# Kernel optimization log

Hardware: AMD Instinct MI355X
Metric: run time of the kernel (lower is better)

## Reference

```python
import jax, jax.numpy as jnp
import numpy as np

VOCAB, EMBED, HIDDEN = 32000, 256, 1024
B, T = 64, 256


def setup_inputs() -> dict:
    key = jax.random.key(0)
    ks = jax.random.split(key, 8)
    s = 0.05
    return {
        "x": jax.random.randint(ks[0], (B, T), 0, VOCAB),
        "embed_table": jax.random.normal(ks[1], (VOCAB, EMBED), jnp.float32) * s,
        "W_ih": jax.random.normal(ks[2], (4 * HIDDEN, EMBED), jnp.float32) * s,
        "W_hh": jax.random.normal(ks[3], (4 * HIDDEN, HIDDEN), jnp.float32) * s,
        "b_ih": jax.random.normal(ks[4], (4 * HIDDEN,), jnp.float32) * s,
        "b_hh": jax.random.normal(ks[5], (4 * HIDDEN,), jnp.float32) * s,
        "fc_W": jax.random.normal(ks[6], (VOCAB, HIDDEN), jnp.float32) * s,
        "fc_b": jax.random.normal(ks[7], (VOCAB,), jnp.float32) * s,
    }


def _lstm_last_hidden(emb, W_ih, W_hh, b_ih, b_hh):
    # emb: [B, T, E]. PyTorch gate order: i, f, g, o.
    H = W_hh.shape[1]
    # Precompute input-side gate projections for all steps: [T, B, 4H]
    x_gates = jnp.einsum('bte,ge->tbg', emb, W_ih) + (b_ih + b_hh)

    def step(carry, xg):
        h, c = carry
        z = xg + h @ W_hh.T  # [B, 4H]
        i = jax.nn.sigmoid(z[:, 0 * H:1 * H])
        f = jax.nn.sigmoid(z[:, 1 * H:2 * H])
        g = jnp.tanh(z[:, 2 * H:3 * H])
        o = jax.nn.sigmoid(z[:, 3 * H:4 * H])
        c = f * c + i * g
        h = o * jnp.tanh(c)
        return (h, c), None

    bsz = emb.shape[0]
    h0 = jnp.zeros((bsz, H), emb.dtype)
    (h, _), _ = jax.lax.scan(step, (h0, h0), x_gates)
    return h  # last hidden state [B, H]


def reference(x, embed_table, W_ih, W_hh, b_ih, b_hh, fc_W, fc_b):
    emb = embed_table[x]  # [B, T, E]
    h_last = _lstm_last_hidden(emb, W_ih, W_hh, b_ih, b_hh)
    return h_last @ fc_W.T + fc_b  # [B, VOCAB]
```

## Files before the change

### kernel.cpp

```cpp
#include <hip/hip_runtime.h>
#include <hip/hip_bf16.h>

#define VOCAB  32000
#define EMBED  256
#define HIDDEN 1024
#define G4     4096
#define BATCH  64
#define SEQ    256

typedef short s16x8 __attribute__((ext_vector_type(8)));
typedef float f32x4 __attribute__((ext_vector_type(4)));

static __device__ __forceinline__ unsigned short f2bf(float f) {
    unsigned u = __float_as_uint(f);
    unsigned r = (u + 0x7fffu + ((u >> 16) & 1u)) >> 16;
    return (unsigned short)r;
}
static __device__ __forceinline__ float bf2f(unsigned short s) {
    return __uint_as_float(((unsigned)s) << 16);
}

__global__ __launch_bounds__(256) void lstm_wprep(
    const float* __restrict__ W_hh,
    unsigned short* __restrict__ Wf)
{
    const int tile = blockIdx.x;
    const int ky   = blockIdx.y;
    const int tid  = threadIdx.x;
    const int wv   = tid >> 6;
    const int lane = tid & 63;
    const int ks   = ky * 4 + wv;
    const int r    = lane & 15;
    const int g    = lane >> 4;
    const int grow = (r >> 2) * 1024 + tile * 4 + (r & 3);
    const float* src = W_hh + (long)grow * 1024 + ks * 32 + g * 8;

    s16x8 hi, lo;
#pragma unroll
    for (int e = 0; e < 8; ++e) {
        const float v = src[e];
        const unsigned short h = f2bf(v);
        hi[e] = (short)h;
        lo[e] = (short)f2bf(v - bf2f(h));
    }
    s16x8* dst = (s16x8*)(Wf + ((long)(tile * 32 + ks) * 2) * 512) + lane;
    dst[0]  = hi;
    dst[64] = lo;
}

__global__ __launch_bounds__(256) void lstm_xgates(
    const int* __restrict__ x,
    const float* __restrict__ emb,
    const float* __restrict__ W_ih,
    const float* __restrict__ b_ih,
    const float* __restrict__ b_hh,
    float* __restrict__ xgT)
{
    const int t   = blockIdx.y;
    const int n0  = blockIdx.x * 64;
    const int tid = threadIdx.x;
    const int ty  = tid >> 4;
    const int tx  = tid & 15;

    __shared__ float As[64][36];
    __shared__ float Bs[64][36];
    __shared__ int   ridx[64];

    if (tid < 64) ridx[tid] = x[tid * SEQ + t];
    __syncthreads();

    float acc[4][4];
#pragma unroll
    for (int i = 0; i < 4; ++i)
#pragma unroll
        for (int j = 0; j < 4; ++j) acc[i][j] = 0.f;

    const int lr = tid >> 2;
    const int lc = (tid & 3) * 8;
    const float* abase = W_ih + (long)(n0 + lr) * EMBED + lc;
    const float* bbase = emb + (long)ridx[lr] * EMBED + lc;

    for (int k0 = 0; k0 < EMBED; k0 += 32) {
        *(float4*)&As[lr][lc]     = *(const float4*)(abase + k0);
        *(float4*)&As[lr][lc + 4] = *(const float4*)(abase + k0 + 4);
        *(float4*)&Bs[lr][lc]     = *(const float4*)(bbase + k0);
        *(float4*)&Bs[lr][lc + 4] = *(const float4*)(bbase + k0 + 4);
        __syncthreads();

#pragma unroll
        for (int kk = 0; kk < 32; kk += 4) {
            float4 av[4], bv[4];
#pragma unroll
            for (int i = 0; i < 4; ++i) av[i] = *(const float4*)&As[ty + 16 * i][kk];
#pragma unroll
            for (int j = 0; j < 4; ++j) bv[j] = *(const float4*)&Bs[tx + 16 * j][kk];
#pragma unroll
            for (int i = 0; i < 4; ++i)
#pragma unroll
                for (int j = 0; j < 4; ++j)
                    acc[i][j] += av[i].x * bv[j].x + av[i].y * bv[j].y
                               + av[i].z * bv[j].z + av[i].w * bv[j].w;
        }
        __syncthreads();
    }

#pragma unroll
    for (int i = 0; i < 4; ++i) {
        const int n = n0 + ty + 16 * i;
        const float bias = b_ih[n] + b_hh[n];
#pragma unroll
        for (int j = 0; j < 4; ++j) {
            const int b = tx + 16 * j;
            xgT[((long)t * G4 + n) * BATCH + b] = acc[i][j] + bias;
        }
    }
}

__global__ void lstm_init(float* __restrict__ c,
                          unsigned short* __restrict__ hhi,
                          unsigned short* __restrict__ hlo)
{
    const int i = blockIdx.x * blockDim.x + threadIdx.x;
    if (i < BATCH * HIDDEN) { c[i] = 0.f; hhi[i] = 0; hlo[i] = 0; }
}

__global__ __launch_bounds__(512, 1) void lstm_step(
    const unsigned short* __restrict__ Wf,
    const float* __restrict__ xgT_t,
    const unsigned short* __restrict__ hHi_in,
    const unsigned short* __restrict__ hLo_in,
    unsigned short* __restrict__ hHi_out,
    unsigned short* __restrict__ hLo_out,
    float* __restrict__ c)
{
    const int tile = blockIdx.x;
    const int tid  = threadIdx.x;
    const int w    = __builtin_amdgcn_readfirstlane(tid >> 6);
    const int lane = tid & 63;
    const int r16  = lane & 15;
    const int g    = lane >> 4;

    __shared__ float Zs[8 * 16 * 66];

    const s16x8* Wf8 = (const s16x8*)Wf;
    const s16x8* hh8 = (const s16x8*)hHi_in;
    const s16x8* hl8 = (const s16x8*)hLo_in;

    s16x8 Whi[4], Wlo[4];
#pragma unroll
    for (int s = 0; s < 4; ++s) {
        const long bi = ((long)(tile * 32 + w * 4 + s) * 2) * 64 + lane;
        Whi[s] = Wf8[bi];
        Wlo[s] = Wf8[bi + 64];
    }

    float xgv[4] = {0.f, 0.f, 0.f, 0.f};
    if (w < 4) {
#pragma unroll
        for (int gg = 0; gg < 4; ++gg)
            xgv[gg] = xgT_t[((long)(gg << 10) + (tile << 2) + w) * BATCH + lane];
    }

    f32x4 acc[4];
#pragma unroll
    for (int m = 0; m < 4; ++m) acc[m] = (f32x4){0.f, 0.f, 0.f, 0.f};

    s16x8 ah[2][4], al[2][4];
#pragma unroll
    for (int m = 0; m < 4; ++m) {
        const int hidx = (m * 16 + r16) * 128 + (w * 4) * 4 + g;
        ah[0][m] = hh8[hidx];
        al[0][m] = hl8[hidx];
    }

#pragma unroll
    for (int s = 0; s < 4; ++s) {
        const int cur = s & 1, nxt = cur ^ 1;
        if (s < 3) {
#pragma unroll
            for (int m = 0; m < 4; ++m) {
                const int hidx = (m * 16 + r16) * 128 + (w * 4 + s + 1) * 4 + g;
                ah[nxt][m] = hh8[hidx];
                al[nxt][m] = hl8[hidx];
            }
        }
#pragma unroll
        for (int m = 0; m < 4; ++m) {
            acc[m] = __builtin_amdgcn_mfma_f32_16x16x32_bf16(ah[cur][m], Whi[s], acc[m], 0, 0, 0);
            acc[m] = __builtin_amdgcn_mfma_f32_16x16x32_bf16(al[cur][m], Whi[s], acc[m], 0, 0, 0);
            acc[m] = __builtin_amdgcn_mfma_f32_16x16x32_bf16(ah[cur][m], Wlo[s], acc[m], 0, 0, 0);
        }
    }

#pragma unroll
    for (int m = 0; m < 4; ++m)
#pragma unroll
        for (int q = 0; q < 4; ++q) {
            const int b = m * 16 + g * 4 + q;
            Zs[(w * 16 + r16) * 66 + b] = acc[m][q];
        }
    __syncthreads();

    if (w < 4) {
        const int jj = w;
        const int b  = lane;
        float z[4];
#pragma unroll
        for (int gg = 0; gg < 4; ++gg) {
            float sum = xgv[gg];
#pragma unroll
            for (int wp = 0; wp < 8; ++wp)
                sum += Zs[(wp * 16 + gg * 4 + jj) * 66 + b];
            z[gg] = sum;
        }
        const float ig = 1.f / (1.f + __expf(-z[0]));
        const float fg = 1.f / (1.f + __expf(-z[1]));
        const float gt = tanhf(z[2]);
        const float og = 1.f / (1.f + __expf(-z[3]));
        float* cp = c + (tile * 64 + b) * 4 + jj;
        const float cn = fg * (*cp) + ig * gt;
        *cp = cn;
        const float hn = og * tanhf(cn);
        const unsigned short hhi = f2bf(hn);
        const unsigned short hlo = f2bf(hn - bf2f(hhi));
        hHi_out[b * HIDDEN + tile * 4 + jj] = hhi;
        hLo_out[b * HIDDEN + tile * 4 + jj] = hlo;
    }
}

__global__ __launch_bounds__(256) void lstm_fc(
    const unsigned short* __restrict__ h_hi,
    const unsigned short* __restrict__ h_lo,
    const float* __restrict__ fc_W,
    const float* __restrict__ fc_b,
    float* __restrict__ out)
{
    const int v0  = blockIdx.x * 64;
    const int tid = threadIdx.x;
    const int ty  = tid >> 4;
    const int tx  = tid & 15;

    __shared__ float Hs[64][36];
    __shared__ float Ws[64][36];

    float acc[4][4];
#pragma unroll
    for (int i = 0; i < 4; ++i)
#pragma unroll
        for (int j = 0; j < 4; ++j) acc[i][j] = 0.f;

    const int lr = tid >> 2;
    const int lc = (tid & 3) * 8;
    const s16x8* hi8 = (const s16x8*)h_hi;
    const s16x8* lo8 = (const s16x8*)h_lo;
    const float* wbase = fc_W + (long)(v0 + lr) * HIDDEN + lc;

    for (int k0 = 0; k0 < HIDDEN; k0 += 32) {
        const int hidx = lr * 128 + ((k0 + lc) >> 3);
        const s16x8 vh = hi8[hidx];
        const s16x8 vl = lo8[hidx];
#pragma unroll
        for (int e = 0; e < 8; ++e)
            Hs[lr][lc + e] = bf2f((unsigned short)vh[e]) + bf2f((unsigned short)vl[e]);
        *(float4*)&Ws[lr][lc]     = *(const float4*)(wbase + k0);
        *(float4*)&Ws[lr][lc + 4] = *(const float4*)(wbase + k0 + 4);
        __syncthreads();

#pragma unroll
        for (int kk = 0; kk < 32; kk += 4) {
            float4 hv[4], wv[4];
#pragma unroll
            for (int i = 0; i < 4; ++i) hv[i] = *(const float4*)&Hs[ty + 16 * i][kk];
#pragma unroll
            for (int j = 0; j < 4; ++j) wv[j] = *(const float4*)&Ws[tx + 16 * j][kk];
#pragma unroll
            for (int i = 0; i < 4; ++i)
#pragma unroll
                for (int j = 0; j < 4; ++j)
                    acc[i][j] += hv[i].x * wv[j].x + hv[i].y * wv[j].y
                               + hv[i].z * wv[j].z + hv[i].w * wv[j].w;
        }
        __syncthreads();
    }

#pragma unroll
    for (int j = 0; j < 4; ++j) {
        const int v = v0 + tx + 16 * j;
        const float bias = fc_b[v];
#pragma unroll
        for (int i = 0; i < 4; ++i) {
            const int b = ty + 16 * i;
            out[(long)b * VOCAB + v] = acc[i][j] + bias;
        }
    }
}

extern "C" void kernel_launch(void* const* d_in, const int* in_sizes, int n_in,
                              void* d_out, int out_size, void* d_ws, size_t ws_size,
                              hipStream_t stream)
{
    const int*   x     = (const int*)d_in[0];
    const float* emb   = (const float*)d_in[1];
    const float* W_ih  = (const float*)d_in[2];
    const float* W_hh  = (const float*)d_in[3];
    const float* b_ih  = (const float*)d_in[4];
    const float* b_hh  = (const float*)d_in[5];
    const float* fc_W  = (const float*)d_in[6];
    const float* fc_b  = (const float*)d_in[7];
    float* out = (float*)d_out;

    float* xgT = (float*)d_ws;
    unsigned short* Wf   = (unsigned short*)(xgT + (long)SEQ * G4 * BATCH);
    unsigned short* hHiA = Wf + (long)256 * 32 * 2 * 512;
    unsigned short* hLoA = hHiA + BATCH * HIDDEN;
    unsigned short* hHiB = hLoA + BATCH * HIDDEN;
    unsigned short* hLoB = hHiB + BATCH * HIDDEN;
    float* c = (float*)(hLoB + BATCH * HIDDEN);

    lstm_wprep<<<dim3(256, 8), 256, 0, stream>>>(W_hh, Wf);
    lstm_xgates<<<dim3(G4 / 64, SEQ), 256, 0, stream>>>(x, emb, W_ih, b_ih, b_hh, xgT);
    lstm_init<<<dim3(BATCH * HIDDEN / 256), 256, 0, stream>>>(c, hHiA, hLoA);

    unsigned short* hhi[2] = {hHiA, hHiB};
    unsigned short* hlo[2] = {hLoA, hLoB};
    for (int t = 0; t < SEQ; ++t) {
        lstm_step<<<dim3(HIDDEN / 4), 512, 0, stream>>>(
            Wf, xgT + (long)t * G4 * BATCH,
            hhi[t & 1], hlo[t & 1], hhi[(t + 1) & 1], hlo[(t + 1) & 1], c);
    }
    lstm_fc<<<dim3(VOCAB / 64), 256, 0, stream>>>(hHiA, hLoA, fc_W, fc_b, out);
}
```

Measured before the change: 4.006 ms.

## Replace per-timestep kernel launches with one persistent cooperative LSTM kernel

The 256 separate lstm_step launches become one cooperative kernel that loops over timesteps and uses grid.sync between steps. The cell state stays in registers instead of global memory, and the init kernel is folded into the persistent kernel. This removes per-launch overhead and the global c read/write each step. In exchange it adds the cost of a grid-wide barrier per step and needs all 256 blocks to be co-resident.

```diff
diff --git a/kernel.cpp b/kernel.cpp
--- a/kernel.cpp
+++ b/kernel.cpp
@@ -1,5 +1,8 @@
 #include <hip/hip_runtime.h>
 #include <hip/hip_bf16.h>
+#include <hip/hip_cooperative_groups.h>
+
+namespace cg = cooperative_groups;
 
 #define VOCAB  32000
 #define EMBED  256
@@ -116,23 +119,14 @@
     }
 }
 
-__global__ void lstm_init(float* __restrict__ c,
-                          unsigned short* __restrict__ hhi,
-                          unsigned short* __restrict__ hlo)
-{
-    const int i = blockIdx.x * blockDim.x + threadIdx.x;
-    if (i < BATCH * HIDDEN) { c[i] = 0.f; hhi[i] = 0; hlo[i] = 0; }
-}
-
-__global__ __launch_bounds__(512, 1) void lstm_step(
+__global__ __launch_bounds__(512, 2) void lstm_persist(
     const unsigned short* __restrict__ Wf,
-    const float* __restrict__ xgT_t,
-    const unsigned short* __restrict__ hHi_in,
-    const unsigned short* __restrict__ hLo_in,
-    unsigned short* __restrict__ hHi_out,
-    unsigned short* __restrict__ hLo_out,
-    float* __restrict__ c)
-{
+    const float* __restrict__ xgT,
+    unsigned short* hHiA, unsigned short* hLoA,
+    unsigned short* hHiB, unsigned short* hLoB)
+{
+    cg::grid_group grid = cg::this_grid();
+
     const int tile = blockIdx.x;
     const int tid  = threadIdx.x;
     const int w    = __builtin_amdgcn_readfirstlane(tid >> 6);
@@ -143,8 +137,6 @@
     __shared__ float Zs[8 * 16 * 66];
 
     const s16x8* Wf8 = (const s16x8*)Wf;
-    const s16x8* hh8 = (const s16x8*)hHi_in;
-    const s16x8* hl8 = (const s16x8*)hLo_in;
 
     s16x8 Whi[4], Wlo[4];
 #pragma unroll
@@ -154,77 +146,94 @@
         Wlo[s] = Wf8[bi + 64];
     }
 
-    float xgv[4] = {0.f, 0.f, 0.f, 0.f};
     if (w < 4) {
-#pragma unroll
-        for (int gg = 0; gg < 4; ++gg)
-            xgv[gg] = xgT_t[((long)(gg << 10) + (tile << 2) + w) * BATCH + lane];
-    }
-
-    f32x4 acc[4];
-#pragma unroll
-    for (int m = 0; m < 4; ++m) acc[m] = (f32x4){0.f, 0.f, 0.f, 0.f};
-
-    s16x8 ah[2][4], al[2][4];
-#pragma unroll
-    for (int m = 0; m < 4; ++m) {
-        const int hidx = (m * 16 + r16) * 128 + (w * 4) * 4 + g;
-        ah[0][m] = hh8[hidx];
-        al[0][m] = hl8[hidx];
-    }
-
-#pragma unroll
-    for (int s = 0; s < 4; ++s) {
-        const int cur = s & 1, nxt = cur ^ 1;
-        if (s < 3) {
+        hHiA[lane * HIDDEN + tile * 4 + w] = 0;
+        hLoA[lane * HIDDEN + tile * 4 + w] = 0;
+    }
+    float creg = 0.f;
+
+    grid.sync();
+
+    for (int t = 0; t < SEQ; ++t) {
+        const s16x8* hh8 = (const s16x8*)((t & 1) ? hHiB : hHiA);
+        const s16x8* hl8 = (const s16x8*)((t & 1) ? hLoB : hLoA);
+        unsigned short* ohi = (t & 1) ? hHiA : hHiB;
+        unsigned short* olo = (t & 1) ? hLoA : hLoB;
+        const float* xgt = xgT + (long)t * G4 * BATCH;
+
+        float xgv[4];
+        if (w < 4) {
+#pragma unroll
+            for (int gg = 0; gg < 4; ++gg)
+                xgv[gg] = xgt[((long)(gg << 10) + (tile << 2) + w) * BATCH + lane];
+        }
+
+        f32x4 acc[4];
+#pragma unroll
+        for (int m = 0; m < 4; ++m) acc[m] = (f32x4){0.f, 0.f, 0.f, 0.f};
+
+        s16x8 ah[2][4], al[2][4];
+#pragma unroll
+        for (int m = 0; m < 4; ++m) {
+            const int hidx = (m * 16 + r16) * 128 + (w * 4) * 4 + g;
+            ah[0][m] = hh8[hidx];
+            al[0][m] = hl8[hidx];
+        }
+
+#pragma unroll
+        for (int s = 0; s < 4; ++s) {
+            const int cur = s & 1, nxt = cur ^ 1;
+            if (s < 3) {
+#pragma unroll
+                for (int m = 0; m < 4; ++m) {
+                    const int hidx = (m * 16 + r16) * 128 + (w * 4 + s + 1) * 4 + g;
+                    ah[nxt][m] = hh8[hidx];
+                    al[nxt][m] = hl8[hidx];
+                }
+            }
 #pragma unroll
             for (int m = 0; m < 4; ++m) {
-                const int hidx = (m * 16 + r16) * 128 + (w * 4 + s + 1) * 4 + g;
-                ah[nxt][m] = hh8[hidx];
-                al[nxt][m] = hl8[hidx];
+                acc[m] = __builtin_amdgcn_mfma_f32_16x16x32_bf16(ah[cur][m], Whi[s], acc[m], 0, 0, 0);
+                acc[m] = __builtin_amdgcn_mfma_f32_16x16x32_bf16(al[cur][m], Whi[s], acc[m], 0, 0, 0);
+                acc[m] = __builtin_amdgcn_mfma_f32_16x16x32_bf16(ah[cur][m], Wlo[s], acc[m], 0, 0, 0);
             }
         }
-#pragma unroll
-        for (int m = 0; m < 4; ++m) {
-            acc[m] = __builtin_amdgcn_mfma_f32_16x16x32_bf16(ah[cur][m], Whi[s], acc[m], 0, 0, 0);
-            acc[m] = __builtin_amdgcn_mfma_f32_16x16x32_bf16(al[cur][m], Whi[s], acc[m], 0, 0, 0);
-            acc[m] = __builtin_amdgcn_mfma_f32_16x16x32_bf16(ah[cur][m], Wlo[s], acc[m], 0, 0, 0);
-        }
-    }
-
-#pragma unroll
-    for (int m = 0; m < 4; ++m)
-#pragma unroll
-        for (int q = 0; q < 4; ++q) {
-            const int b = m * 16 + g * 4 + q;
-            Zs[(w * 16 + r16) * 66 + b] = acc[m][q];
-        }
-    __syncthreads();
-
-    if (w < 4) {
-        const int jj = w;
-        const int b  = lane;
-        float z[4];
-#pragma unroll
-        for (int gg = 0; gg < 4; ++gg) {
-            float sum = xgv[gg];
-#pragma unroll
-            for (int wp = 0; wp < 8; ++wp)
-                sum += Zs[(wp * 16 + gg * 4 + jj) * 66 + b];
-            z[gg] = sum;
-        }
-        const float ig = 1.f / (1.f + __expf(-z[0]));
-        const float fg = 1.f / (1.f + __expf(-z[1]));
-        const float gt = tanhf(z[2]);
-        const float og = 1.f / (1.f + __expf(-z[3]));
-        float* cp = c + (tile * 64 + b) * 4 + jj;
-        const float cn = fg * (*cp) + ig * gt;
-        *cp = cn;
-        const float hn = og * tanhf(cn);
-        const unsigned short hhi = f2bf(hn);
-        const unsigned short hlo = f2bf(hn - bf2f(hhi));
-        hHi_out[b * HIDDEN + tile * 4 + jj] = hhi;
-        hLo_out[b * HIDDEN + tile * 4 + jj] = hlo;
+
+#pragma unroll
+        for (int m = 0; m < 4; ++m)
+#pragma unroll
+            for (int q = 0; q < 4; ++q) {
+                const int b = m * 16 + g * 4 + q;
+                Zs[(w * 16 + r16) * 66 + b] = acc[m][q];
+            }
+        __syncthreads();
+
+        if (w < 4) {
+            const int jj = w;
+            const int b  = lane;
+            float z[4];
+#pragma unroll
+            for (int gg = 0; gg < 4; ++gg) {
+                float sum = xgv[gg];
+#pragma unroll
+                for (int wp = 0; wp < 8; ++wp)
+                    sum += Zs[(wp * 16 + gg * 4 + jj) * 66 + b];
+                z[gg] = sum;
+            }
+            const float ig = 1.f / (1.f + __expf(-z[0]));
+            const float fg = 1.f / (1.f + __expf(-z[1]));
+            const float gt = tanhf(z[2]);
+            const float og = 1.f / (1.f + __expf(-z[3]));
+            const float cn = fg * creg + ig * gt;
+            creg = cn;
+            const float hn = og * tanhf(cn);
+            const unsigned short hhi = f2bf(hn);
+            const unsigned short hlo = f2bf(hn - bf2f(hhi));
+            ohi[b * HIDDEN + tile * 4 + jj] = hhi;
+            olo[b * HIDDEN + tile * 4 + jj] = hlo;
+        }
+
+        grid.sync();
     }
 }
 
@@ -315,18 +324,14 @@
     unsigned short* hLoA = hHiA + BATCH * HIDDEN;
     unsigned short* hHiB = hLoA + BATCH * HIDDEN;
     unsigned short* hLoB = hHiB + BATCH * HIDDEN;
-    float* c = (float*)(hLoB + BATCH * HIDDEN);
 
     lstm_wprep<<<dim3(256, 8), 256, 0, stream>>>(W_hh, Wf);
     lstm_xgates<<<dim3(G4 / 64, SEQ), 256, 0, stream>>>(x, emb, W_ih, b_ih, b_hh, xgT);
-    lstm_init<<<dim3(BATCH * HIDDEN / 256), 256, 0, stream>>>(c, hHiA, hLoA);
-
-    unsigned short* hhi[2] = {hHiA, hHiB};
-    unsigned short* hlo[2] = {hLoA, hLoB};
-    for (int t = 0; t < SEQ; ++t) {
-        lstm_step<<<dim3(HIDDEN / 4), 512, 0, stream>>>(
-            Wf, xgT + (long)t * G4 * BATCH,
-            hhi[t & 1], hlo[t & 1], hhi[(t + 1) & 1], hlo[(t + 1) & 1], c);
-    }
+
+    void* args[] = {(void*)&Wf, (void*)&xgT,
+                    (void*)&hHiA, (void*)&hLoA, (void*)&hHiB, (void*)&hLoB};
+    hipLaunchCooperativeKernel((void*)lstm_persist, dim3(256), dim3(512),
+                               args, 0, stream);
+
     lstm_fc<<<dim3(VOCAB / 64), 256, 0, stream>>>(hHiA, hLoA, fc_W, fc_b, out);
 }
```

Result: slower. 12.10 ms (+202.0%).
